# Kernel tuning notes

Hardware: AMD Instinct MI355X
Metric: run time of the kernel (lower is better)

The kernel has to match this reference:

```python
import jax, jax.numpy as jnp
import numpy as np

B, S, D = 2, 2048, 1024
H, HD = 16, 64          # num_heads, head_dim = dim_feedforward // num_heads
ROPE_BASE = 10000.0


def _apply_rope(t):
    # t: [b, h, s, hd] -> RoPE applied over last dim, positions = token index
    b, h, s, hd = t.shape
    theta = 1.0 / (ROPE_BASE ** (jnp.arange(0, hd, 2, dtype=jnp.float32) / hd))  # [hd/2]
    ang = jnp.arange(s, dtype=jnp.float32)[:, None] * theta[None, :]             # [s, hd/2]
    cos, sin = jnp.cos(ang), jnp.sin(ang)
    tr = t.reshape(b, h, s, hd // 2, 2)
    t0, t1 = tr[..., 0], tr[..., 1]
    o0 = t0 * cos - t1 * sin
    o1 = t1 * cos + t0 * sin
    return jnp.stack([o0, o1], axis=-1).reshape(b, h, s, hd)


def setup_inputs() -> dict:
    key = jax.random.key(0)
    ks = jax.random.split(key, 8)
    x = jax.random.normal(ks[0], (B, S, D), dtype=jnp.float32)
    wq = jax.random.normal(ks[1], (D, H * HD), dtype=jnp.float32) * 0.02
    wk = jax.random.normal(ks[2], (D, H * HD), dtype=jnp.float32) * 0.02
    wv = jax.random.normal(ks[3], (D, H * HD), dtype=jnp.float32) * 0.02
    bq = jax.random.normal(ks[4], (H * HD,), dtype=jnp.float32) * 0.02
    bk = jax.random.normal(ks[5], (H * HD,), dtype=jnp.float32) * 0.02
    bv = jax.random.normal(ks[6], (H * HD,), dtype=jnp.float32) * 0.02
    # trailing padding per batch; valid_len large enough that every causal+history
    # window contains at least one unpadded key (valid_len > S - max_history)
    valid_len = jax.random.randint(ks[7], (B,), S - 256, S + 1)
    key_padding_mask = (jnp.arange(S)[None, :] >= valid_len[:, None]).astype(jnp.int32)
    return {"x": x, "wq": wq, "bq": bq, "wk": wk, "bk": bk, "wv": wv, "bv": bv,
            "key_padding_mask": key_padding_mask, "max_history_len": 512}


def reference(x, wq, bq, wk, bk, wv, bv, key_padding_mask, max_history_len):
    b, s, d = x.shape
    scale = HD ** (-0.5)
    q = (x @ wq + bq).reshape(b, s, H, HD).transpose(0, 2, 1, 3)  # [b,h,s,hd]
    k = (x @ wk + bk).reshape(b, s, H, HD).transpose(0, 2, 1, 3)
    v = (x @ wv + bv).reshape(b, s, H, HD).transpose(0, 2, 1, 3)
    q = _apply_rope(q)
    k = _apply_rope(k)
    scores = jnp.einsum('bhqd,bhkd->bhqk', q, k) * scale          # [b,h,s,s]
    i = jnp.arange(s)[:, None]
    j = jnp.arange(s)[None, :]
    band = (j <= i) & ((i - j) <= (max_history_len - 1))          # causal + history
    allowed = band[None, None, :, :] & (key_padding_mask == 0)[:, None, None, :]
    scores = jnp.where(allowed, scores, -jnp.inf)
    attn = jax.nn.softmax(scores, axis=-1)
    out = jnp.einsum('bhqk,bhkd->bhqd', attn, v)                  # [b,h,s,hd]
    return out.transpose(0, 2, 1, 3).reshape(b, s, H * HD)
```

## Files before the change

kernel.cpp:

```cpp
#include <hip/hip_runtime.h>
#include <hip/hip_bf16.h>
#include <stdint.h>


typedef __attribute__((ext_vector_type(8))) short bf16x8;
typedef __attribute__((ext_vector_type(4))) short bf16x4;
typedef __attribute__((ext_vector_type(4))) float f32x4;

#define DEV __device__ __forceinline__

DEV ushort f2b(float f) {
  union { float f; uint32_t u; } v; v.f = f;
  uint32_t r = v.u + 0x7FFFu + ((v.u >> 16) & 1u);
  return (ushort)(r >> 16);
}
DEV float b2f(ushort u) {
  union { uint32_t u; float f; } v; v.u = ((uint32_t)u) << 16;
  return v.f;
}
DEV uint cvt_pk_bf16(float lo, float hi) {
  uint r;
  asm("v_cvt_pk_bf16_f32 %0, %1, %2" : "=v"(r) : "v"(lo), "v"(hi));
  return r;
}
DEV float fast_exp2(float x) {
#if __has_builtin(__builtin_amdgcn_exp2f)
  return __builtin_amdgcn_exp2f(x);
#else
  return exp2f(x);
#endif
}

DEV void gload_lds16(const void* g, void* l) {
  __builtin_amdgcn_global_load_lds((const __attribute__((address_space(1))) void*)g,
                                   (__attribute__((address_space(3))) void*)l,
                                   16, 0, 0);
}

__global__ __launch_bounds__(256) void prep_x_kernel(const float* __restrict__ x,
                                                     ushort* __restrict__ xb) {
  int t = blockIdx.x * 256 + threadIdx.x;
  float4 v = ((const float4*)x)[t];
  bf16x4 o;
  o[0] = (short)f2b(v.x); o[1] = (short)f2b(v.y);
  o[2] = (short)f2b(v.z); o[3] = (short)f2b(v.w);
  *(bf16x4*)&xb[(size_t)t * 4] = o;
}

__global__ void prep_w_kernel(const float* __restrict__ wq, const float* __restrict__ wk,
                              const float* __restrict__ wv, ushort* __restrict__ wt) {
  __shared__ float tile[32][33];
  int which = blockIdx.z;
  const float* w = which == 0 ? wq : (which == 1 ? wk : wv);
  int n0 = blockIdx.x * 32, k0 = blockIdx.y * 32;
  tile[threadIdx.y][threadIdx.x] = w[(size_t)(k0 + threadIdx.y) * 1024 + n0 + threadIdx.x];
  __syncthreads();
  wt[((size_t)which * 1024 + n0 + threadIdx.y) * 1024 + k0 + threadIdx.x] =
      f2b(tile[threadIdx.x][threadIdx.y]);
}

__global__ __launch_bounds__(256) void rope_tab_kernel(float2* __restrict__ tab) {
  int t = blockIdx.x * 256 + threadIdx.x;
  int i = t & 31, s = t >> 5;
  float theta = powf(10000.0f, -(float)i / 32.0f);
  float ang = (float)s * theta;
  tab[t] = make_float2(cosf(ang), sinf(ang));
}

__global__ __launch_bounds__(512, 2) void qkv_gemm_kernel(
    const ushort* __restrict__ A, const ushort* __restrict__ Bt,
    const float* __restrict__ bq, const float* __restrict__ bk,
    const float* __restrict__ bv, const float2* __restrict__ tab,
    ushort* __restrict__ qb, ushort* __restrict__ kb, ushort* __restrict__ vt) {
  const int K = 1024;
  __shared__ alignas(16) ushort sA[2][256 * 64];
  __shared__ alignas(16) ushort sB[2][192 * 64];

  int tid = threadIdx.x;
  int lane = tid & 63;
  int lhi = lane >> 4, llo = lane & 15;
  int wid = tid >> 6;
  int wr = wid >> 2, wc = wid & 3;

  int id = blockIdx.x;
  int wg = (id & 7) * 32 + (id >> 3);
  int bm = wg >> 4, bn = wg & 15;

  const ushort* Abase = A + (size_t)bm * 256 * K;
  const ushort* Bbase = Bt + (size_t)bn * 192 * K;

  f32x4 acc[8][3];
#pragma unroll
  for (int i = 0; i < 8; ++i)
#pragma unroll
    for (int j = 0; j < 3; ++j) acc[i][j] = (f32x4){0.f, 0.f, 0.f, 0.f};

  auto stage = [&](int kt, int bb) {
    int k0 = kt * 64;
#pragma unroll
    for (int c = 0; c < 4; ++c) {
      int idx = c * 512 + tid;
      int row = idx >> 3, gslot = (idx & 7) ^ (row & 7);
      gload_lds16(Abase + (size_t)row * K + k0 + gslot * 8, &sA[bb][(idx & ~63) * 8]);
    }
#pragma unroll
    for (int c = 0; c < 3; ++c) {
      int idx = c * 512 + tid;
      int row = idx >> 3, gslot = (idx & 7) ^ (row & 7);
      gload_lds16(Bbase + (size_t)row * K + k0 + gslot * 8, &sB[bb][(idx & ~63) * 8]);
    }
  };

  stage(0, 0); stage(1, 1);

  for (int kt = 0; kt < 16; ++kt) {
    if (kt < 15) asm volatile("s_waitcnt vmcnt(7)" ::: "memory");
    else         asm volatile("s_waitcnt vmcnt(0)" ::: "memory");
    __builtin_amdgcn_sched_barrier(0);
    __builtin_amdgcn_s_barrier();
    __builtin_amdgcn_sched_barrier(0);

    int buf = kt & 1;
    const ushort* pA = sA[buf];
    const ushort* pB = sB[buf];

    bf16x8 bfr[3][2], af[4][2];
#pragma unroll
    for (int nf = 0; nf < 3; ++nf) {
      int r = wc * 48 + nf * 16 + llo;
#pragma unroll
      for (int ks = 0; ks < 2; ++ks)
        bfr[nf][ks] = *(const bf16x8*)&pB[r * 64 + (((ks * 4 + lhi) ^ (r & 7)) * 8)];
    }
#pragma unroll
    for (int mf = 0; mf < 4; ++mf) {
      int r = wr * 128 + mf * 16 + llo;
#pragma unroll
      for (int ks = 0; ks < 2; ++ks)
        af[mf][ks] = *(const bf16x8*)&pA[r * 64 + (((ks * 4 + lhi) ^ (r & 7)) * 8)];
    }
    __builtin_amdgcn_s_setprio(1);
#pragma unroll
    for (int mf = 0; mf < 4; ++mf)
#pragma unroll
      for (int nf = 0; nf < 3; ++nf)
#pragma unroll
        for (int ks = 0; ks < 2; ++ks)
          acc[mf][nf] = __builtin_amdgcn_mfma_f32_16x16x32_bf16(bfr[nf][ks], af[mf][ks], acc[mf][nf], 0, 0, 0);
    __builtin_amdgcn_s_setprio(0);
    __builtin_amdgcn_sched_barrier(0);
    __builtin_amdgcn_s_barrier();
    __builtin_amdgcn_sched_barrier(0);

#pragma unroll
    for (int mf = 0; mf < 4; ++mf) {
      int r = wr * 128 + (4 + mf) * 16 + llo;
#pragma unroll
      for (int ks = 0; ks < 2; ++ks)
        af[mf][ks] = *(const bf16x8*)&pA[r * 64 + (((ks * 4 + lhi) ^ (r & 7)) * 8)];
    }
    asm volatile("s_waitcnt lgkmcnt(0)" ::: "memory");
    __builtin_amdgcn_sched_barrier(0);
    __builtin_amdgcn_s_barrier();
    __builtin_amdgcn_sched_barrier(0);
    if (kt + 2 < 16) stage(kt + 2, buf);
    __builtin_amdgcn_s_setprio(1);
#pragma unroll
    for (int mf = 0; mf < 4; ++mf)
#pragma unroll
      for (int nf = 0; nf < 3; ++nf)
#pragma unroll
        for (int ks = 0; ks < 2; ++ks)
          acc[4 + mf][nf] = __builtin_amdgcn_mfma_f32_16x16x32_bf16(bfr[nf][ks], af[mf][ks], acc[4 + mf][nf], 0, 0, 0);
    __builtin_amdgcn_s_setprio(0);
    __builtin_amdgcn_sched_barrier(0);
  }

  const float SCL = 0.18033688011112042f;
#pragma unroll
  for (int mf = 0; mf < 8; ++mf) {
    int m = bm * 256 + wr * 128 + mf * 16 + llo;
    int s = m & 2047, bidx = m >> 11;
#pragma unroll
    for (int nf = 0; nf < 3; ++nf) {
      int nbase = bn * 192 + wc * 48 + nf * 16;
      int n0 = nbase + lhi * 4;
      f32x4 a = acc[mf][nf];
      if (nbase < 1024) {
        float4 cs = *(const float4*)&tab[s * 32 + ((n0 & 63) >> 1)];
        float4 bb = *(const float4*)&bq[n0];
        float t0 = a[0] + bb.x, t1 = a[1] + bb.y;
        float t2 = a[2] + bb.z, t3 = a[3] + bb.w;
        uint2 ov;
        ov.x = cvt_pk_bf16((t0 * cs.x - t1 * cs.y) * SCL, (t1 * cs.x + t0 * cs.y) * SCL);
        ov.y = cvt_pk_bf16((t2 * cs.z - t3 * cs.w) * SCL, (t3 * cs.z + t2 * cs.w) * SCL);
        int h = n0 >> 6;
        *(uint2*)&qb[((size_t)(bidx * 16 + h) * 2048 + s) * 64 + (n0 & 63)] = ov;
      } else if (nbase < 2048) {
        float4 cs = *(const float4*)&tab[s * 32 + ((n0 & 63) >> 1)];
        float4 bb = *(const float4*)&bk[n0 - 1024];
        float t0 = a[0] + bb.x, t1 = a[1] + bb.y;
        float t2 = a[2] + bb.z, t3 = a[3] + bb.w;
        uint2 ov;
        ov.x = cvt_pk_bf16(t0 * cs.x - t1 * cs.y, t1 * cs.x + t0 * cs.y);
        ov.y = cvt_pk_bf16(t2 * cs.z - t3 * cs.w, t3 * cs.z + t2 * cs.w);
        int h = (n0 >> 6) & 15;
        *(uint2*)&kb[((size_t)(bidx * 16 + h) * 2048 + s) * 64 + (n0 & 63)] = ov;
      } else {
        float4 bb = *(const float4*)&bv[n0 - 2048];
        int hd_g = n0 - 2048;
        int h = hd_g >> 6, hd = hd_g & 63;
        size_t vb = ((size_t)(bidx * 16 + h) * 64 + hd) * 2048 + s;
        vt[vb]        = f2b(a[0] + bb.x);
        vt[vb + 2048] = f2b(a[1] + bb.y);
        vt[vb + 4096] = f2b(a[2] + bb.z);
        vt[vb + 6144] = f2b(a[3] + bb.w);
      }
    }
  }
}

__global__ __launch_bounds__(512) void attn_kernel(
    const ushort* __restrict__ qb, const ushort* __restrict__ kb,
    const ushort* __restrict__ vt, const int* __restrict__ kmask,
    const int* __restrict__ whist, float* __restrict__ out) {
  __shared__ alignas(16) ushort sK[128 * 64];
  __shared__ alignas(16) ushort sV[64 * 136];
  __shared__ alignas(16) uint   sPd[8][16 * 68];

  int tid = threadIdx.x;
  int lane = tid & 63, wid = tid >> 6;
  int lhi = lane >> 4, llo = lane & 15;

  int id = blockIdx.x;
  int xcd = id & 7, sub = id >> 3;
  int bh = xcd * 4 + (sub >> 4);
  int qtile = sub & 15;
  int b = bh >> 4;
  int q0 = qtile * 128;
  int qw0 = q0 + wid * 16;
  int W = *whist;

  const ushort* qptr = qb + (size_t)bh * 2048 * 64;
  const ushort* kptr = kb + (size_t)bh * 2048 * 64;
  const ushort* vptr = vt + (size_t)bh * 64 * 2048;
  const int* mrow = kmask + b * 2048;

  bf16x8 qf0, qf1;
  {
    size_t base = (size_t)(qw0 + llo) * 64 + lhi * 8;
    qf0 = *(const bf16x8*)&qptr[base];
    qf1 = *(const bf16x8*)&qptr[base + 32];
  }

  float m_ = -1e4f, l_ = 0.f;
  f32x4 o[4];
#pragma unroll
  for (int nf = 0; nf < 4; ++nf) o[nf] = (f32x4){0.f, 0.f, 0.f, 0.f};

  int lo = q0 - (W - 1); if (lo < 0) lo = 0;
  int jt0 = lo & ~127;
  int nt = ((q0 + 128) - jt0) >> 7;

  bf16x8 kreg[2], vreg[2];
  int mreg0, mreg1;
  int krow = tid >> 2, kslot2 = (tid & 3) * 2;
  int vrow = tid >> 3, vslot2 = (tid & 7) * 2;

  auto load_tile = [&](int jt) {
    kreg[0] = *(const bf16x8*)&kptr[(size_t)(jt + krow) * 64 + kslot2 * 8];
    kreg[1] = *(const bf16x8*)&kptr[(size_t)(jt + krow) * 64 + (kslot2 + 1) * 8];
    vreg[0] = *(const bf16x8*)&vptr[(size_t)vrow * 2048 + jt + vslot2 * 8];
    vreg[1] = *(const bf16x8*)&vptr[(size_t)vrow * 2048 + jt + (vslot2 + 1) * 8];
    mreg0 = mrow[jt + lane];
    mreg1 = mrow[jt + 64 + lane];
  };

  load_tile(jt0);
  for (int it = 0; it < nt; ++it) {
    int jt = jt0 + it * 128;
    __syncthreads();
    *(bf16x8*)&sK[krow * 64 + ((kslot2 ^ (krow & 7)) * 8)] = kreg[0];
    *(bf16x8*)&sK[krow * 64 + (((kslot2 + 1) ^ (krow & 7)) * 8)] = kreg[1];
    *(bf16x8*)&sV[vrow * 136 + vslot2 * 8] = vreg[0];
    *(bf16x8*)&sV[vrow * 136 + (vslot2 + 1) * 8] = vreg[1];
    unsigned long long pm0 = __ballot(mreg0 != 0);
    unsigned long long pm1 = __ballot(mreg1 != 0);
    if (it + 1 < nt) load_tile(jt + 128);
    __syncthreads();

    bool active = (jt <= qw0 + 15) && (jt + 127 >= qw0 - W + 1);
    if (active) {
      f32x4 sc[8];
#pragma unroll
      for (int kb8 = 0; kb8 < 8; ++kb8) sc[kb8] = (f32x4){0.f, 0.f, 0.f, 0.f};
      __builtin_amdgcn_s_setprio(1);
#pragma unroll
      for (int ks = 0; ks < 2; ++ks) {
        bf16x8 qq = ks ? qf1 : qf0;
#pragma unroll
        for (int kb8 = 0; kb8 < 8; ++kb8) {
          int r = kb8 * 16 + llo;
          bf16x8 kf = *(const bf16x8*)&sK[r * 64 + (((ks * 4 + lhi) ^ (r & 7)) * 8)];
          sc[kb8] = __builtin_amdgcn_mfma_f32_16x16x32_bf16(kf, qq, sc[kb8], 0, 0, 0);
        }
      }
      __builtin_amdgcn_s_setprio(0);

      bool fastp = (jt + 127 <= qw0) && (jt >= qw0 + 16 - W) &&
                   (pm0 == 0ull) && (pm1 == 0ull);
      if (!fastp) {
        int qi = qw0 + llo;
#pragma unroll
        for (int kb8 = 0; kb8 < 8; ++kb8) {
          uint nib = (uint)((kb8 < 4 ? pm0 : pm1) >> ((kb8 & 3) * 16 + lhi * 4)) & 0xFu;
#pragma unroll
          for (int j = 0; j < 4; ++j) {
            int key = jt + kb8 * 16 + lhi * 4 + j;
            bool k_ok = (key <= qi) && (qi - key < W) && !((nib >> j) & 1u);
            sc[kb8][j] = k_ok ? sc[kb8][j] : -1e30f;
          }
        }
      }

      float tm[8];
#pragma unroll
      for (int kb8 = 0; kb8 < 8; ++kb8)
        tm[kb8] = fmaxf(fmaxf(sc[kb8][0], sc[kb8][1]), fmaxf(sc[kb8][2], sc[kb8][3]));
      float t = fmaxf(fmaxf(fmaxf(tm[0], tm[1]), fmaxf(tm[2], tm[3])),
                      fmaxf(fmaxf(tm[4], tm[5]), fmaxf(tm[6], tm[7])));
      t = fmaxf(t, __shfl_xor(t, 16));
      t = fmaxf(t, __shfl_xor(t, 32));

      if (t > m_ + 8.f) {
        float fac = fast_exp2(m_ - t);
        l_ *= fac;
#pragma unroll
        for (int nf = 0; nf < 4; ++nf) o[nf] *= fac;
        m_ = t;
      }

      float sm[8];
#pragma unroll
      for (int kb8 = 0; kb8 < 8; ++kb8) {
#pragma unroll
        for (int j = 0; j < 4; ++j) sc[kb8][j] = fast_exp2(sc[kb8][j] - m_);
        sm[kb8] = (sc[kb8][0] + sc[kb8][1]) + (sc[kb8][2] + sc[kb8][3]);
      }
      float ps = ((sm[0] + sm[1]) + (sm[2] + sm[3])) + ((sm[4] + sm[5]) + (sm[6] + sm[7]));
      ps += __shfl_xor(ps, 16);
      ps += __shfl_xor(ps, 32);
      l_ += ps;

      uint* prow = &sPd[wid][llo * 68];
#pragma unroll
      for (int kb8 = 0; kb8 < 8; ++kb8) {
        uint2 d;
        d.x = cvt_pk_bf16(sc[kb8][0], sc[kb8][1]);
        d.y = cvt_pk_bf16(sc[kb8][2], sc[kb8][3]);
        *(uint2*)&prow[kb8 * 8 + lhi * 2] = d;
      }
      bf16x8 pf[4];
#pragma unroll
      for (int ksb = 0; ksb < 4; ++ksb)
        pf[ksb] = *(const bf16x8*)&sPd[wid][llo * 68 + ksb * 16 + lhi * 4];

      __builtin_amdgcn_s_setprio(1);
#pragma unroll
      for (int nf = 0; nf < 4; ++nf) {
#pragma unroll
        for (int ksb = 0; ksb < 4; ++ksb) {
          bf16x8 vf = *(const bf16x8*)&sV[(nf * 16 + llo) * 136 + ksb * 32 + lhi * 8];
          o[nf] = __builtin_amdgcn_mfma_f32_16x16x32_bf16(vf, pf[ksb], o[nf], 0, 0, 0);
        }
      }
      __builtin_amdgcn_s_setprio(0);
    }
  }

  float inv = 1.f / l_;
  int qi = qw0 + llo;
  size_t obase = ((size_t)b * 2048 + qi) * 1024 + (bh & 15) * 64 + lhi * 4;
#pragma unroll
  for (int nf = 0; nf < 4; ++nf) {
    float4 st = make_float4(o[nf][0] * inv, o[nf][1] * inv, o[nf][2] * inv, o[nf][3] * inv);
    *(float4*)&out[obase + nf * 16] = st;
  }
}

extern "C" void kernel_launch(void* const* d_in, const int* in_sizes, int n_in,
                              void* d_out, int out_size, void* d_ws, size_t ws_size,
                              hipStream_t stream) {
  const float* x  = (const float*)d_in[0];
  const float* wq = (const float*)d_in[1];
  const float* bq = (const float*)d_in[2];
  const float* wk = (const float*)d_in[3];
  const float* bk = (const float*)d_in[4];
  const float* wv = (const float*)d_in[5];
  const float* bv = (const float*)d_in[6];
  const int* kmask = (const int*)d_in[7];
  const int* whist = (const int*)d_in[8];
  float* out = (float*)d_out;

  char* ws = (char*)d_ws;
  ushort* xb  = (ushort*)(ws);
  ushort* wt  = (ushort*)(ws + (8ull  << 20));
  ushort* qb  = (ushort*)(ws + (14ull << 20));
  ushort* kb  = (ushort*)(ws + (22ull << 20));
  ushort* vt  = (ushort*)(ws + (30ull << 20));
  float2* tab = (float2*)(ws + (38ull << 20));

  prep_x_kernel<<<4096, 256, 0, stream>>>(x, xb);
  prep_w_kernel<<<dim3(32, 32, 3), dim3(32, 32, 1), 0, stream>>>(wq, wk, wv, wt);
  rope_tab_kernel<<<256, 256, 0, stream>>>(tab);
  qkv_gemm_kernel<<<256, 512, 0, stream>>>(xb, wt, bq, bk, bv, tab, qb, kb, vt);
  attn_kernel<<<512, 512, 0, stream>>>(qb, kb, vt, kmask, whist, out);
}
```

Measured before the change: 77.90 us.

## Merge prep kernels into one launch and retile QKV GEMM to 128x128

The three preprocessing kernels (x cast, weight transpose-cast, RoPE table) are combined into a single launch indexed by block range, and the weight transpose now uses float4 loads and 4-wide bf16 stores. The QKV GEMM moves from 256x192 tiles with 512 threads (256 blocks) to 128x128 tiles with 256 threads (768 blocks). This aims to cut launch overhead and fill the GPU's CUs better, at the cost of less operand reuse per tile and more total global and LDS traffic.

```diff
diff --git a/kernel.cpp b/kernel.cpp
--- a/kernel.cpp
+++ b/kernel.cpp
@@ -37,75 +37,82 @@
                                    16, 0, 0);
 }
 
-__global__ __launch_bounds__(256) void prep_x_kernel(const float* __restrict__ x,
-                                                     ushort* __restrict__ xb) {
-  int t = blockIdx.x * 256 + threadIdx.x;
-  float4 v = ((const float4*)x)[t];
-  bf16x4 o;
-  o[0] = (short)f2b(v.x); o[1] = (short)f2b(v.y);
-  o[2] = (short)f2b(v.z); o[3] = (short)f2b(v.w);
-  *(bf16x4*)&xb[(size_t)t * 4] = o;
-}
-
-__global__ void prep_w_kernel(const float* __restrict__ wq, const float* __restrict__ wk,
-                              const float* __restrict__ wv, ushort* __restrict__ wt) {
-  __shared__ float tile[32][33];
-  int which = blockIdx.z;
-  const float* w = which == 0 ? wq : (which == 1 ? wk : wv);
-  int n0 = blockIdx.x * 32, k0 = blockIdx.y * 32;
-  tile[threadIdx.y][threadIdx.x] = w[(size_t)(k0 + threadIdx.y) * 1024 + n0 + threadIdx.x];
-  __syncthreads();
-  wt[((size_t)which * 1024 + n0 + threadIdx.y) * 1024 + k0 + threadIdx.x] =
-      f2b(tile[threadIdx.x][threadIdx.y]);
-}
-
-__global__ __launch_bounds__(256) void rope_tab_kernel(float2* __restrict__ tab) {
-  int t = blockIdx.x * 256 + threadIdx.x;
-  int i = t & 31, s = t >> 5;
-  float theta = powf(10000.0f, -(float)i / 32.0f);
-  float ang = (float)s * theta;
-  tab[t] = make_float2(cosf(ang), sinf(ang));
-}
-
-__global__ __launch_bounds__(512, 2) void qkv_gemm_kernel(
+__global__ __launch_bounds__(256) void prep_kernel(
+    const float* __restrict__ x, ushort* __restrict__ xb,
+    const float* __restrict__ wq, const float* __restrict__ wk,
+    const float* __restrict__ wv, ushort* __restrict__ wt,
+    float2* __restrict__ tab) {
+  int bid = blockIdx.x, tid = threadIdx.x;
+  if (bid < 4096) {
+    int t = bid * 256 + tid;
+    float4 v = ((const float4*)x)[t];
+    bf16x4 o;
+    o[0] = (short)f2b(v.x); o[1] = (short)f2b(v.y);
+    o[2] = (short)f2b(v.z); o[3] = (short)f2b(v.w);
+    *(bf16x4*)&xb[(size_t)t * 4] = o;
+  } else if (bid < 4352) {
+    int t = (bid - 4096) * 256 + tid;
+    int i = t & 31, s = t >> 5;
+    float theta = powf(10000.0f, -(float)i / 32.0f);
+    float ang = (float)s * theta;
+    tab[t] = make_float2(cosf(ang), sinf(ang));
+  } else {
+    __shared__ float tile[32][33];
+    int rem = bid - 4352;
+    int which = rem >> 10, t2 = rem & 1023;
+    int n0 = (t2 & 31) * 32, k0 = (t2 >> 5) * 32;
+    const float* w = which == 0 ? wq : (which == 1 ? wk : wv);
+    int r = tid >> 3, c4 = (tid & 7) * 4;
+    float4 v = *(const float4*)&w[(size_t)(k0 + r) * 1024 + n0 + c4];
+    tile[r][c4] = v.x; tile[r][c4 + 1] = v.y;
+    tile[r][c4 + 2] = v.z; tile[r][c4 + 3] = v.w;
+    __syncthreads();
+    bf16x4 o;
+#pragma unroll
+    for (int i = 0; i < 4; ++i) o[i] = (short)f2b(tile[c4 + i][r]);
+    *(bf16x4*)&wt[((size_t)(which * 1024 + n0 + r)) * 1024 + k0 + c4] = o;
+  }
+}
+
+__global__ __launch_bounds__(256, 2) void qkv_gemm_kernel(
     const ushort* __restrict__ A, const ushort* __restrict__ Bt,
     const float* __restrict__ bq, const float* __restrict__ bk,
     const float* __restrict__ bv, const float2* __restrict__ tab,
     ushort* __restrict__ qb, ushort* __restrict__ kb, ushort* __restrict__ vt) {
   const int K = 1024;
-  __shared__ alignas(16) ushort sA[2][256 * 64];
-  __shared__ alignas(16) ushort sB[2][192 * 64];
+  __shared__ alignas(16) ushort sA[2][128 * 64];
+  __shared__ alignas(16) ushort sB[2][128 * 64];
 
   int tid = threadIdx.x;
   int lane = tid & 63;
   int lhi = lane >> 4, llo = lane & 15;
   int wid = tid >> 6;
-  int wr = wid >> 2, wc = wid & 3;
+  int wr = wid >> 1, wc = wid & 1;
 
   int id = blockIdx.x;
-  int wg = (id & 7) * 32 + (id >> 3);
-  int bm = wg >> 4, bn = wg & 15;
-
-  const ushort* Abase = A + (size_t)bm * 256 * K;
-  const ushort* Bbase = Bt + (size_t)bn * 192 * K;
-
-  f32x4 acc[8][3];
-#pragma unroll
-  for (int i = 0; i < 8; ++i)
-#pragma unroll
-    for (int j = 0; j < 3; ++j) acc[i][j] = (f32x4){0.f, 0.f, 0.f, 0.f};
+  int wg = (id & 7) * 96 + (id >> 3);
+  int bm = wg / 24, bn = wg % 24;
+
+  const ushort* Abase = A + (size_t)bm * 128 * K;
+  const ushort* Bbase = Bt + (size_t)bn * 128 * K;
+
+  f32x4 acc[4][4];
+#pragma unroll
+  for (int i = 0; i < 4; ++i)
+#pragma unroll
+    for (int j = 0; j < 4; ++j) acc[i][j] = (f32x4){0.f, 0.f, 0.f, 0.f};
 
   auto stage = [&](int kt, int bb) {
     int k0 = kt * 64;
 #pragma unroll
     for (int c = 0; c < 4; ++c) {
-      int idx = c * 512 + tid;
+      int idx = c * 256 + tid;
       int row = idx >> 3, gslot = (idx & 7) ^ (row & 7);
       gload_lds16(Abase + (size_t)row * K + k0 + gslot * 8, &sA[bb][(idx & ~63) * 8]);
     }
 #pragma unroll
-    for (int c = 0; c < 3; ++c) {
-      int idx = c * 512 + tid;
+    for (int c = 0; c < 4; ++c) {
+      int idx = c * 256 + tid;
       int row = idx >> 3, gslot = (idx & 7) ^ (row & 7);
       gload_lds16(Bbase + (size_t)row * K + k0 + gslot * 8, &sB[bb][(idx & ~63) * 8]);
     }
@@ -114,7 +121,7 @@
   stage(0, 0); stage(1, 1);
 
   for (int kt = 0; kt < 16; ++kt) {
-    if (kt < 15) asm volatile("s_waitcnt vmcnt(7)" ::: "memory");
+    if (kt < 15) asm volatile("s_waitcnt vmcnt(8)" ::: "memory");
     else         asm volatile("s_waitcnt vmcnt(0)" ::: "memory");
     __builtin_amdgcn_sched_barrier(0);
     __builtin_amdgcn_s_barrier();
@@ -124,26 +131,26 @@
     const ushort* pA = sA[buf];
     const ushort* pB = sB[buf];
 
-    bf16x8 bfr[3][2], af[4][2];
-#pragma unroll
-    for (int nf = 0; nf < 3; ++nf) {
-      int r = wc * 48 + nf * 16 + llo;
+    bf16x8 bfr[4][2], af[2][2];
+#pragma unroll
+    for (int nf = 0; nf < 4; ++nf) {
+      int r = wc * 64 + nf * 16 + llo;
 #pragma unroll
       for (int ks = 0; ks < 2; ++ks)
         bfr[nf][ks] = *(const bf16x8*)&pB[r * 64 + (((ks * 4 + lhi) ^ (r & 7)) * 8)];
     }
 #pragma unroll
-    for (int mf = 0; mf < 4; ++mf) {
-      int r = wr * 128 + mf * 16 + llo;
+    for (int mf = 0; mf < 2; ++mf) {
+      int r = wr * 64 + mf * 16 + llo;
 #pragma unroll
       for (int ks = 0; ks < 2; ++ks)
         af[mf][ks] = *(const bf16x8*)&pA[r * 64 + (((ks * 4 + lhi) ^ (r & 7)) * 8)];
     }
     __builtin_amdgcn_s_setprio(1);
 #pragma unroll
-    for (int mf = 0; mf < 4; ++mf)
-#pragma unroll
-      for (int nf = 0; nf < 3; ++nf)
+    for (int mf = 0; mf < 2; ++mf)
+#pragma unroll
+      for (int nf = 0; nf < 4; ++nf)
 #pragma unroll
         for (int ks = 0; ks < 2; ++ks)
           acc[mf][nf] = __builtin_amdgcn_mfma_f32_16x16x32_bf16(bfr[nf][ks], af[mf][ks], acc[mf][nf], 0, 0, 0);
@@ -153,8 +160,8 @@
     __builtin_amdgcn_sched_barrier(0);
 
 #pragma unroll
-    for (int mf = 0; mf < 4; ++mf) {
-      int r = wr * 128 + (4 + mf) * 16 + llo;
+    for (int mf = 0; mf < 2; ++mf) {
+      int r = wr * 64 + (2 + mf) * 16 + llo;
 #pragma unroll
       for (int ks = 0; ks < 2; ++ks)
         af[mf][ks] = *(const bf16x8*)&pA[r * 64 + (((ks * 4 + lhi) ^ (r & 7)) * 8)];
@@ -166,24 +173,24 @@
     if (kt + 2 < 16) stage(kt + 2, buf);
     __builtin_amdgcn_s_setprio(1);
 #pragma unroll
-    for (int mf = 0; mf < 4; ++mf)
-#pragma unroll
-      for (int nf = 0; nf < 3; ++nf)
+    for (int mf = 0; mf < 2; ++mf)
+#pragma unroll
+      for (int nf = 0; nf < 4; ++nf)
 #pragma unroll
         for (int ks = 0; ks < 2; ++ks)
-          acc[4 + mf][nf] = __builtin_amdgcn_mfma_f32_16x16x32_bf16(bfr[nf][ks], af[mf][ks], acc[4 + mf][nf], 0, 0, 0);
+          acc[2 + mf][nf] = __builtin_amdgcn_mfma_f32_16x16x32_bf16(bfr[nf][ks], af[mf][ks], acc[2 + mf][nf], 0, 0, 0);
     __builtin_amdgcn_s_setprio(0);
     __builtin_amdgcn_sched_barrier(0);
   }
 
   const float SCL = 0.18033688011112042f;
 #pragma unroll
-  for (int mf = 0; mf < 8; ++mf) {
-    int m = bm * 256 + wr * 128 + mf * 16 + llo;
+  for (int mf = 0; mf < 4; ++mf) {
+    int m = bm * 128 + wr * 64 + mf * 16 + llo;
     int s = m & 2047, bidx = m >> 11;
 #pragma unroll
-    for (int nf = 0; nf < 3; ++nf) {
-      int nbase = bn * 192 + wc * 48 + nf * 16;
+    for (int nf = 0; nf < 4; ++nf) {
+      int nbase = bn * 128 + wc * 64 + nf * 16;
       int n0 = nbase + lhi * 4;
       f32x4 a = acc[mf][nf];
       if (nbase < 1024) {
@@ -410,9 +417,7 @@
   ushort* vt  = (ushort*)(ws + (30ull << 20));
   float2* tab = (float2*)(ws + (38ull << 20));
 
-  prep_x_kernel<<<4096, 256, 0, stream>>>(x, xb);
-  prep_w_kernel<<<dim3(32, 32, 3), dim3(32, 32, 1), 0, stream>>>(wq, wk, wv, wt);
-  rope_tab_kernel<<<256, 256, 0, stream>>>(tab);
-  qkv_gemm_kernel<<<256, 512, 0, stream>>>(xb, wt, bq, bk, bv, tab, qb, kb, vt);
+  prep_kernel<<<7424, 256, 0, stream>>>(x, xb, wq, wk, wv, wt, tab);
+  qkv_gemm_kernel<<<768, 256, 0, stream>>>(xb, wt, bq, bk, bv, tab, qb, kb, vt);
   attn_kernel<<<512, 512, 0, stream>>>(qb, kb, vt, kmask, whist, out);
 }
```

New measurement: 82.38 us. 1.06x slower.
